# Performance work log

Measured on AMD Instinct MI355X. Metric: run time of the kernel, lower is better.

The kernel has to match this reference:

```python
import jax, jax.numpy as jnp
import numpy as np

DIM = 512; H = 56; W = 56; HEADS = 16; WS = 7; SHIFT = 3; MLP_RATIO = 4.0; B = 16
N = WS * WS              # tokens per window = 49
NW = (H // WS) * (W // WS)  # 64 windows
HID = int(DIM * MLP_RATIO)


def _rel_pos_index():
    coords = np.stack(np.meshgrid(np.arange(WS), np.arange(WS), indexing='ij')).reshape(2, -1)
    rel = (coords[:, :, None] - coords[:, None, :]).transpose(1, 2, 0)
    rel[..., 0] += WS - 1
    rel[..., 1] += WS - 1
    rel[..., 0] *= 2 * WS - 1
    return rel.sum(-1).astype(np.int32)  # (N, N)


def _attn_mask():
    # standard SW-MSA mask: 0 within same region, -100 across regions
    img = np.zeros((H, W), np.float32)
    cnt = 0
    sl = (slice(0, -WS), slice(-WS, -SHIFT), slice(-SHIFT, None))
    for hs in sl:
        for ws_ in sl:
            img[hs, ws_] = cnt
            cnt += 1
    mw = img.reshape(H // WS, WS, W // WS, WS).transpose(0, 2, 1, 3).reshape(-1, N)  # (NW, N)
    am = mw[:, None, :] - mw[:, :, None]
    return np.where(am != 0, np.float32(-100.0), np.float32(0.0))  # (NW, N, N)


def setup_inputs() -> dict:
    key = jax.random.key(0)
    ks = jax.random.split(key, 6)
    s = jnp.float32(0.02)
    return {
        'x': jax.random.normal(ks[0], (B, H * W, DIM), jnp.float32),
        'qkv_w': jax.random.normal(ks[1], (3 * DIM, DIM), jnp.float32) * s,  # layout (h dh 3) x C
        'qkv_b': jnp.zeros((3 * DIM,), jnp.float32),
        'out_w': jax.random.normal(ks[2], (DIM, DIM), jnp.float32) * s,
        'out_b': jnp.zeros((DIM,), jnp.float32),
        'rp_bias_table': jax.random.normal(ks[3], ((2 * WS - 1) ** 2, HEADS), jnp.float32) * s,
        'fc1_w': jax.random.normal(ks[4], (HID, DIM), jnp.float32) * s,
        'fc1_b': jnp.zeros((HID,), jnp.float32),
        'fc2_w': jax.random.normal(ks[5], (DIM, HID), jnp.float32) * s,
        'fc2_b': jnp.zeros((DIM,), jnp.float32),
        'ln1_w': jnp.ones((DIM,), jnp.float32),
        'ln1_b': jnp.zeros((DIM,), jnp.float32),
        'ln2_w': jnp.ones((DIM,), jnp.float32),
        'ln2_b': jnp.zeros((DIM,), jnp.float32),
        'attn_mask': jnp.asarray(_attn_mask()),
        'rp_index': jnp.asarray(_rel_pos_index()),
    }


def _ln(x, w, b):
    m = x.mean(-1, keepdims=True)
    v = ((x - m) ** 2).mean(-1, keepdims=True)
    return (x - m) * jax.lax.rsqrt(v + 1e-5) * w + b


def reference(x, qkv_w, qkv_b, out_w, out_b, rp_bias_table, fc1_w, fc1_b, fc2_w, fc2_b,
              ln1_w, ln1_b, ln2_w, ln2_b, attn_mask, rp_index):
    Bx, L, C = x.shape
    dh = C // HEADS
    scale = jnp.float32(dh) ** -0.5

    shortcut = x
    y = _ln(x, ln1_w, ln1_b).reshape(Bx, H, W, C)
    y = jnp.roll(y, (-SHIFT, -SHIFT), axis=(1, 2))
    # window partition -> (B*NW, N, C)
    xw = y.reshape(Bx, H // WS, WS, W // WS, WS, C).transpose(0, 1, 3, 2, 4, 5).reshape(-1, N, C)

    qkv = (xw @ qkv_w.T + qkv_b).reshape(-1, N, HEADS, dh, 3).transpose(4, 0, 2, 1, 3)
    q, k, v = qkv[0] * scale, qkv[1], qkv[2]          # (B_, h, N, dh)
    attn = jnp.einsum('bhnd,bhmd->bhnm', q, k)        # (B_, h, N, N)

    bias = rp_bias_table[rp_index.reshape(-1)].reshape(N, N, HEADS).transpose(2, 0, 1)
    attn = attn + 2.0 * bias                          # source adds the bias twice (faithful)
    attn = attn.reshape(Bx, NW, HEADS, N, N) + attn_mask[None, :, None]
    attn = jax.nn.softmax(attn, axis=-1).reshape(-1, HEADS, N, N)

    o = jnp.einsum('bhnm,bhmd->bhnd', attn, v).transpose(0, 2, 1, 3).reshape(-1, N, C)
    o = o @ out_w.T + out_b
    # window reverse + roll back
    o = o.reshape(Bx, H // WS, W // WS, WS, WS, C).transpose(0, 1, 3, 2, 4, 5).reshape(Bx, H, W, C)
    o = jnp.roll(o, (SHIFT, SHIFT), axis=(1, 2)).reshape(Bx, L, C)

    x = shortcut + o
    h2 = _ln(x, ln2_w, ln2_b)
    h2 = jax.nn.gelu(h2 @ fc1_w.T + fc1_b, approximate=False) @ fc2_w.T + fc2_b
    return x + h2
```

## Files before the change

kernel.cpp:

```cpp
#include <hip/hip_runtime.h>
#include <hip/hip_bf16.h>

#define CDIM 512
#define NHEADS 16
#define DH 32
#define NTOK 49
#define NWIN 64
#define BATCH 16
#define HH 56
#define WW 56
#define LTOK 3136
#define TTOK 50176
#define HID 2048
#define SHIFT_ 3

typedef short bf16x8 __attribute__((ext_vector_type(8)));
typedef float f32x4 __attribute__((ext_vector_type(4)));

__device__ __forceinline__ float b2f(unsigned int u) {
    return __uint_as_float((u & 0xffffu) << 16);
}
__device__ __forceinline__ unsigned short f2b(float f) {
    __hip_bfloat16 h = __float2bfloat16(f);
    return *reinterpret_cast<unsigned short*>(&h);
}
__device__ __forceinline__ void load8(const unsigned short* p, float* f) {
    uint4 r = *reinterpret_cast<const uint4*>(p);
    f[0] = b2f(r.x); f[1] = b2f(r.x >> 16);
    f[2] = b2f(r.y); f[3] = b2f(r.y >> 16);
    f[4] = b2f(r.z); f[5] = b2f(r.z >> 16);
    f[6] = b2f(r.w); f[7] = b2f(r.w >> 16);
}
__device__ __forceinline__ uint4 pack8(const float* f) {
    uint4 r;
    r.x = (unsigned)f2b(f[0]) | ((unsigned)f2b(f[1]) << 16);
    r.y = (unsigned)f2b(f[2]) | ((unsigned)f2b(f[3]) << 16);
    r.z = (unsigned)f2b(f[4]) | ((unsigned)f2b(f[5]) << 16);
    r.w = (unsigned)f2b(f[6]) | ((unsigned)f2b(f[7]) << 16);
    return r;
}
__device__ __forceinline__ bool probe_f32(const unsigned* p) { return p[0] == 0x3F800000u; }
__device__ __forceinline__ float ld1(const void* p, size_t i, bool f32) {
    return f32 ? ((const float*)p)[i] : b2f(((const unsigned short*)p)[i]);
}
__device__ __forceinline__ void load8_any(const void* p, size_t idx, bool f32, float* f) {
    if (f32) {
        const float4* q = (const float4*)((const float*)p + idx);
        float4 a = q[0], b = q[1];
        f[0]=a.x; f[1]=a.y; f[2]=a.z; f[3]=a.w; f[4]=b.x; f[5]=b.y; f[6]=b.z; f[7]=b.w;
    } else {
        load8((const unsigned short*)p + idx, f);
    }
}

#define GLOAD_LDS16(g, l) \
    __builtin_amdgcn_global_load_lds( \
        (const __attribute__((address_space(1))) unsigned int*)(g), \
        (__attribute__((address_space(3))) unsigned int*)(l), 16, 0, 0)

__global__ __launch_bounds__(256)
void cvt_kernel(const void* __restrict__ in, unsigned short* __restrict__ out,
                const unsigned* __restrict__ probe)
{
    bool f32in = probe_f32(probe);
    size_t idx = ((size_t)blockIdx.x * 256 + threadIdx.x) * 8;
    float f[8];
    load8_any(in, idx, f32in, f);
    *reinterpret_cast<uint4*>(out + idx) = pack8(f);
}

__global__ __launch_bounds__(256)
void cvt_qkvw_kernel(const void* __restrict__ in, unsigned short* __restrict__ out,
                     const unsigned* __restrict__ probe)
{
    bool f32in = probe_f32(probe);
    int r = blockIdx.x * 4 + (threadIdx.x >> 6);
    int lane = threadIdx.x & 63;
    int s = r >> 9, q = r & 511, h = q >> 5, d = q & 31;
    int orow = h * 96 + d * 3 + s;
    float f[8];
    load8_any(in, (size_t)orow * CDIM + lane * 8, f32in, f);
    *reinterpret_cast<uint4*>(out + (size_t)r * CDIM + lane * 8) = pack8(f);
}

__global__ __launch_bounds__(256)
void cmb_kernel(const void* __restrict__ rp_tab, const int* __restrict__ rp_idx,
                const void* __restrict__ mask, unsigned short* __restrict__ cmb,
                const unsigned* __restrict__ probe)
{
    bool f32in = probe_f32(probe);
    int wh = blockIdx.x;
    int wi = wh >> 4, h = wh & 15;
    for (int e = threadIdx.x; e < 4096; e += 256) {
        int q = e >> 6, k = e & 63;
        float v = -1e30f;
        if (q < NTOK && k < NTOK) {
            int bi = rp_idx[q * NTOK + k];
            v = 2.0f * ld1(rp_tab, (size_t)bi * NHEADS + h, f32in)
              + ld1(mask, (size_t)wi * NTOK * NTOK + (size_t)q * NTOK + k, f32in);
        }
        cmb[(size_t)wh * 4096 + e] = f2b(v);
    }
}

template<int SHIFTED, int XRAW>
__global__ __launch_bounds__(256)
void ln_kernel(const void* __restrict__ xin,
               const void* __restrict__ gw,
               const void* __restrict__ gb,
               unsigned short* __restrict__ out,
               const unsigned* __restrict__ probe)
{
    bool f32in = probe_f32(probe);
    int wid = threadIdx.x >> 6, lane = threadIdx.x & 63;
    int tok = blockIdx.x * 4 + wid;
    int c0 = lane * 8;
    float xs[8];
    load8_any(xin, (size_t)tok * CDIM + c0, XRAW && f32in, xs);
    float s = 0.f, s2 = 0.f;
#pragma unroll
    for (int j = 0; j < 8; ++j) { s += xs[j]; s2 += xs[j] * xs[j]; }
#pragma unroll
    for (int off = 32; off; off >>= 1) { s += __shfl_xor(s, off); s2 += __shfl_xor(s2, off); }
    float mean = s * (1.0f / CDIM);
    float var = s2 * (1.0f / CDIM) - mean * mean;
    float rstd = rsqrtf(var + 1e-5f);
    float wv[8], bv[8], ov[8];
    load8_any(gw, c0, f32in, wv);
    load8_any(gb, c0, f32in, bv);
#pragma unroll
    for (int j = 0; j < 8; ++j) ov[j] = (xs[j] - mean) * rstd * wv[j] + bv[j];
    size_t dst;
    if (SHIFTED) {
        int b = tok / LTOK, l = tok % LTOK;
        int h = l / WW, w = l % WW;
        int hs = (h + HH - SHIFT_) % HH;
        int ws_ = (w + WW - SHIFT_) % WW;
        int wh = hs / 7, ii = hs % 7, wwi = ws_ / 7, jj = ws_ % 7;
        int t = (b * NWIN + wh * 8 + wwi) * NTOK + ii * 7 + jj;
        dst = (size_t)t * CDIM + c0;
    } else {
        dst = (size_t)tok * CDIM + c0;
    }
    *reinterpret_cast<uint4*>(out + dst) = pack8(ov);
}

template<int EPI>
__global__ __launch_bounds__(256)
void gemm_kernel(const unsigned short* __restrict__ A,
                 const unsigned short* __restrict__ Wbf,
                 const void* __restrict__ bias,
                 const void* __restrict__ aux,
                 void* __restrict__ out0,
                 unsigned short* __restrict__ out1,
                 unsigned short* __restrict__ out2,
                 int K, int moff,
                 const unsigned* __restrict__ probe)
{
    bool f32in = probe_f32(probe);
    __shared__ __align__(16) unsigned short sA[2][128 * 32];
    __shared__ __align__(16) unsigned short sB[2][128 * 32];
    int tid = threadIdx.x;
    int wave = tid >> 6, lane = tid & 63, quad = lane >> 4, l16 = lane & 15;
    int bn = blockIdx.x, bm = blockIdx.y;
    int wm = (wave & 1) * 64, wn = (wave >> 1) * 64;

    const unsigned short* aP = A   + (size_t)(bm * 128 + (tid >> 2)) * K + (tid & 3) * 8;
    const unsigned short* bP = Wbf + (size_t)(bn * 128 + (tid >> 2)) * K + (tid & 3) * 8;
    const size_t rowhop = (size_t)64 * K;
    const int loff = tid * 16;

    f32x4 acc[16];
#pragma unroll
    for (int t = 0; t < 16; ++t) acc[t] = (f32x4){0.f, 0.f, 0.f, 0.f};

    GLOAD_LDS16(aP,          (char*)sA[0] + loff);
    GLOAD_LDS16(aP + rowhop, (char*)sA[0] + loff + 4096);
    GLOAD_LDS16(bP,          (char*)sB[0] + loff);
    GLOAD_LDS16(bP + rowhop, (char*)sB[0] + loff + 4096);
    __syncthreads();

    const int NT = K >> 5;
    int cur = 0;
    for (int t = 0; t < NT; ++t) {
        if (t + 1 < NT) {
            int k0 = (t + 1) << 5;
            char* dA = (char*)sA[cur ^ 1] + loff;
            char* dB = (char*)sB[cur ^ 1] + loff;
            GLOAD_LDS16(aP + k0,          dA);
            GLOAD_LDS16(aP + k0 + rowhop, dA + 4096);
            GLOAD_LDS16(bP + k0,          dB);
            GLOAD_LDS16(bP + k0 + rowhop, dB + 4096);
        }
        const unsigned short* cA = sA[cur];
        const unsigned short* cB = sB[cur];
        bf16x8 af[4], bfr[4];
#pragma unroll
        for (int am = 0; am < 4; ++am)
            af[am] = *reinterpret_cast<const bf16x8*>(&cA[(wm + am * 16 + l16) * 32 + quad * 8]);
#pragma unroll
        for (int bn_ = 0; bn_ < 4; ++bn_)
            bfr[bn_] = *reinterpret_cast<const bf16x8*>(&cB[(wn + bn_ * 16 + l16) * 32 + quad * 8]);
#pragma unroll
        for (int am = 0; am < 4; ++am)
#pragma unroll
            for (int bn_ = 0; bn_ < 4; ++bn_)
                acc[am * 4 + bn_] = __builtin_amdgcn_mfma_f32_16x16x32_bf16(
                    af[am], bfr[bn_], acc[am * 4 + bn_], 0, 0, 0);
        __syncthreads();
        cur ^= 1;
    }

#pragma unroll
    for (int bn_ = 0; bn_ < 4; ++bn_) {
        int gn = bn * 128 + wn + bn_ * 16 + l16;
        if (EPI == 0) {
            int s = gn >> 9, h = (gn >> 5) & 15, d = gn & 31;
            float bv = ld1(bias, h * 96 + d * 3 + s, f32in);
            unsigned short* outp = (s == 0) ? (unsigned short*)out0 : (s == 1 ? out1 : out2);
            float mul = (s == 0) ? 0.17677669529663687f : 1.0f;
#pragma unroll
            for (int am = 0; am < 4; ++am) {
#pragma unroll
                for (int r = 0; r < 4; ++r) {
                    int gm = bm * 128 + wm + am * 16 + quad * 4 + r;
                    int w = gm / NTOK, n = gm - w * NTOK;
                    size_t dst = ((size_t)(w * NHEADS + h) * NTOK + n) * DH + d;
                    outp[dst] = f2b((acc[am * 4 + bn_][r] + bv) * mul);
                }
            }
        } else {
            float bv = ld1(bias, gn, f32in);
#pragma unroll
            for (int am = 0; am < 4; ++am) {
#pragma unroll
                for (int r = 0; r < 4; ++r) {
                    int gm = bm * 128 + wm + am * 16 + quad * 4 + r;
                    float v = acc[am * 4 + bn_][r] + bv;
                    if (EPI == 1) {
                        int w = gm / NTOK, n = gm - w * NTOK;
                        int b = w >> 6, wi = w & 63;
                        int wh = wi >> 3, wwi = wi & 7;
                        int ii = n / 7, jj = n - ii * 7;
                        int h_ = (wh * 7 + ii + SHIFT_) % HH;
                        int w_ = (wwi * 7 + jj + SHIFT_) % WW;
                        size_t dst = ((size_t)b * LTOK + h_ * WW + w_) * CDIM + gn;
                        v += ld1(aux, dst, f32in);
                        ((unsigned short*)out0)[dst] = f2b(v);
                    } else if (EPI == 2) {
                        float g = 0.5f * v * (1.0f + erff(v * 0.70710678118654752f));
                        ((unsigned short*)out0)[(size_t)gm * HID + gn] = f2b(g);
                    } else {
                        size_t dst = (size_t)(moff + gm) * CDIM + gn;
                        v += b2f(((const unsigned short*)aux)[dst]);
                        if (f32in) ((float*)out0)[dst] = v;
                        else       ((unsigned short*)out0)[dst] = f2b(v);
                    }
                }
            }
        }
    }
}

__global__ __launch_bounds__(256)
void attn_kernel(const unsigned short* __restrict__ Qb,
                 const unsigned short* __restrict__ Kb,
                 const unsigned short* __restrict__ Vb,
                 const unsigned short* __restrict__ cmb,
                 unsigned short* __restrict__ Ob)
{
    __shared__ __align__(16) unsigned short Pl[4][64 * 72];
    int wid = threadIdx.x >> 6, lane = threadIdx.x & 63;
    int l16 = lane & 15, quad = lane >> 4;
    int wi = blockIdx.x >> 6, rem = blockIdx.x & 63;
    int b = rem >> 2, hq = rem & 3;
    int h = hq * 4 + wid;
    int bw = b * NWIN + wi;
    size_t base = (size_t)(bw * NHEADS + h) * (NTOK * DH);
    const unsigned short* cmbp = cmb + (size_t)(wi * NHEADS + h) * 4096;

    bf16x8 kf[4], qf[4];
#pragma unroll
    for (int t = 0; t < 4; ++t) {
        kf[t] = *reinterpret_cast<const bf16x8*>(Kb + base + (t * 16 + l16) * DH + quad * 8);
        qf[t] = *reinterpret_cast<const bf16x8*>(Qb + base + (t * 16 + l16) * DH + quad * 8);
    }
    f32x4 s[4][4];
#pragma unroll
    for (int kt = 0; kt < 4; ++kt)
#pragma unroll
        for (int nt = 0; nt < 4; ++nt)
            s[kt][nt] = (f32x4){0.f, 0.f, 0.f, 0.f};
#pragma unroll
    for (int kt = 0; kt < 4; ++kt)
#pragma unroll
        for (int nt = 0; nt < 4; ++nt)
            s[kt][nt] = __builtin_amdgcn_mfma_f32_16x16x32_bf16(kf[kt], qf[nt], s[kt][nt], 0, 0, 0);

    float mx[4] = {-1e30f, -1e30f, -1e30f, -1e30f}, sm[4] = {0.f, 0.f, 0.f, 0.f};
#pragma unroll
    for (int kt = 0; kt < 4; ++kt)
#pragma unroll
        for (int nt = 0; nt < 4; ++nt) {
            uint2 cv = *reinterpret_cast<const uint2*>(cmbp + (nt * 16 + l16) * 64 + kt * 16 + quad * 4);
            float c[4] = {b2f(cv.x), b2f(cv.x >> 16), b2f(cv.y), b2f(cv.y >> 16)};
#pragma unroll
            for (int r = 0; r < 4; ++r) {
                float sv = s[kt][nt][r] + c[r];
                s[kt][nt][r] = sv;
                mx[nt] = fmaxf(mx[nt], sv);
            }
        }
#pragma unroll
    for (int nt = 0; nt < 4; ++nt) {
        mx[nt] = fmaxf(mx[nt], __shfl_xor(mx[nt], 16));
        mx[nt] = fmaxf(mx[nt], __shfl_xor(mx[nt], 32));
    }
#pragma unroll
    for (int kt = 0; kt < 4; ++kt)
#pragma unroll
        for (int nt = 0; nt < 4; ++nt)
#pragma unroll
            for (int r = 0; r < 4; ++r) {
                float pv = expf(s[kt][nt][r] - mx[nt]);
                s[kt][nt][r] = pv;
                sm[nt] += pv;
            }
    float rs[4];
#pragma unroll
    for (int nt = 0; nt < 4; ++nt) {
        sm[nt] += __shfl_xor(sm[nt], 16);
        sm[nt] += __shfl_xor(sm[nt], 32);
        rs[nt] = 1.0f / sm[nt];
    }
    unsigned short* P = Pl[wid];
#pragma unroll
    for (int kt = 0; kt < 4; ++kt)
#pragma unroll
        for (int nt = 0; nt < 4; ++nt) {
            uint2 w;
            w.x = (unsigned)f2b(s[kt][nt][0] * rs[nt]) | ((unsigned)f2b(s[kt][nt][1] * rs[nt]) << 16);
            w.y = (unsigned)f2b(s[kt][nt][2] * rs[nt]) | ((unsigned)f2b(s[kt][nt][3] * rs[nt]) << 16);
            *reinterpret_cast<uint2*>(&P[(nt * 16 + l16) * 72 + kt * 16 + quad * 4]) = w;
        }

    f32x4 o[4][2];
#pragma unroll
    for (int mt = 0; mt < 4; ++mt)
#pragma unroll
        for (int n2 = 0; n2 < 2; ++n2)
            o[mt][n2] = (f32x4){0.f, 0.f, 0.f, 0.f};
#pragma unroll
    for (int ks = 0; ks < 2; ++ks) {
        bf16x8 pf[4];
#pragma unroll
        for (int mt = 0; mt < 4; ++mt)
            pf[mt] = *reinterpret_cast<const bf16x8*>(&P[(mt * 16 + l16) * 72 + ks * 32 + quad * 8]);
        bf16x8 vf[2];
#pragma unroll
        for (int n2 = 0; n2 < 2; ++n2) {
            union { bf16x8 v; unsigned short u[8]; } t;
#pragma unroll
            for (int j = 0; j < 8; ++j)
                t.u[j] = Vb[base + (size_t)(ks * 32 + quad * 8 + j) * DH + n2 * 16 + l16];
            vf[n2] = t.v;
        }
#pragma unroll
        for (int mt = 0; mt < 4; ++mt)
#pragma unroll
            for (int n2 = 0; n2 < 2; ++n2)
                o[mt][n2] = __builtin_amdgcn_mfma_f32_16x16x32_bf16(pf[mt], vf[n2], o[mt][n2], 0, 0, 0);
    }
#pragma unroll
    for (int mt = 0; mt < 4; ++mt)
#pragma unroll
        for (int n2 = 0; n2 < 2; ++n2)
#pragma unroll
            for (int r = 0; r < 4; ++r) {
                int q = mt * 16 + quad * 4 + r;
                if (q < NTOK)
                    Ob[((size_t)bw * NTOK + q) * CDIM + h * DH + n2 * 16 + l16] = f2b(o[mt][n2][r]);
            }
}

extern "C" void kernel_launch(void* const* d_in, const int* in_sizes, int n_in,
                              void* d_out, int out_size, void* d_ws, size_t ws_size,
                              hipStream_t stream)
{
    const void* x      = d_in[0];
    const void* qkv_w  = d_in[1];
    const void* qkv_b  = d_in[2];
    const void* out_w  = d_in[3];
    const void* out_b  = d_in[4];
    const void* rp_tab = d_in[5];
    const void* fc1_w  = d_in[6];
    const void* fc1_b  = d_in[7];
    const void* fc2_w  = d_in[8];
    const void* fc2_b  = d_in[9];
    const void* ln1_w  = d_in[10];
    const void* ln1_b  = d_in[11];
    const void* ln2_w  = d_in[12];
    const void* ln2_b  = d_in[13];
    const void* amask  = d_in[14];
    const int*  rp_idx = (const int*)d_in[15];
    const unsigned* probe = (const unsigned*)ln1_w;

    unsigned short* ws = (unsigned short*)d_ws;
    const size_t SZ = (size_t)TTOK * CDIM;
    unsigned short* xw = ws;
    unsigned short* Qb = ws + SZ;
    unsigned short* Kb = ws + 2 * SZ;
    unsigned short* Vb = ws + 3 * SZ;
    unsigned short* Ob = ws + 4 * SZ;
    unsigned short* Cmb = ws;
    unsigned short* X1 = ws;
    unsigned short* Hb = ws + SZ;
    unsigned short* fc1wbf = ws + 3 * SZ;
    unsigned short* fc2wbf = ws + 3 * SZ + (size_t)HID * CDIM;
    unsigned short* L2 = ws + 4 * SZ;
    unsigned short* qkvwbf = (unsigned short*)d_out;
    unsigned short* outwbf = qkvwbf + (size_t)3 * CDIM * CDIM;
    if (ws_size < 5 * SZ * sizeof(unsigned short)) return;

    const int HM = TTOK / 2;

    cvt_qkvw_kernel<<<(3 * CDIM) / 4, 256, 0, stream>>>(qkv_w, qkvwbf, probe);
    cvt_kernel<<<(CDIM * CDIM) / 2048, 256, 0, stream>>>(out_w, outwbf, probe);

    ln_kernel<1, 1><<<TTOK / 4, 256, 0, stream>>>(x, ln1_w, ln1_b, xw, probe);
    gemm_kernel<0><<<dim3((3 * CDIM) / 128, TTOK / 128), 256, 0, stream>>>(
        xw, qkvwbf, qkv_b, nullptr, Qb, Kb, Vb, CDIM, 0, probe);
    cmb_kernel<<<1024, 256, 0, stream>>>(rp_tab, rp_idx, amask, Cmb, probe);
    attn_kernel<<<4096, 256, 0, stream>>>(Qb, Kb, Vb, Cmb, Ob);

    cvt_kernel<<<(HID * CDIM) / 2048, 256, 0, stream>>>(fc1_w, fc1wbf, probe);
    cvt_kernel<<<(HID * CDIM) / 2048, 256, 0, stream>>>(fc2_w, fc2wbf, probe);

    gemm_kernel<1><<<dim3(CDIM / 128, TTOK / 128), 256, 0, stream>>>(
        Ob, outwbf, out_b, x, X1, nullptr, nullptr, CDIM, 0, probe);
    ln_kernel<0, 0><<<TTOK / 4, 256, 0, stream>>>(X1, ln2_w, ln2_b, L2, probe);

    for (int half = 0; half < 2; ++half) {
        size_t mo = (size_t)half * HM;
        gemm_kernel<2><<<dim3(HID / 128, HM / 128), 256, 0, stream>>>(
            L2 + mo * CDIM, fc1wbf, fc1_b, nullptr, Hb, nullptr, nullptr, CDIM, 0, probe);
        gemm_kernel<3><<<dim3(CDIM / 128, HM / 128), 256, 0, stream>>>(
            Hb, fc2wbf, fc2_b, X1, d_out, nullptr, nullptr, HID, (int)mo, probe);
    }
}
```

Before: 1.151 ms.

## Triple-buffer GEMM LDS loads with explicit vmcnt waits and swizzle workgroup order

Moves the GEMM main loop from double to triple buffering in LDS, so each iteration issues loads two K-tiles ahead. The full __syncthreads is replaced by inline s_waitcnt vmcnt(N) plus s_barrier, so only the oldest outstanding stage has to finish. It also remaps block indices so that consecutive workgroups are spread in groups of 8, likely to match the XCD round-robin dispatch and improve L2 locality. This uses more LDS per block, which may reduce occupancy. The hand-written vmcnt counts depend on each thread issuing exactly four loads per stage.

```diff
diff --git a/kernel.cpp b/kernel.cpp
--- a/kernel.cpp
+++ b/kernel.cpp
@@ -158,11 +158,18 @@
                  const unsigned* __restrict__ probe)
 {
     bool f32in = probe_f32(probe);
-    __shared__ __align__(16) unsigned short sA[2][128 * 32];
-    __shared__ __align__(16) unsigned short sB[2][128 * 32];
+    __shared__ __align__(16) unsigned short sA[3][128 * 32];
+    __shared__ __align__(16) unsigned short sB[3][128 * 32];
     int tid = threadIdx.x;
     int wave = tid >> 6, lane = tid & 63, quad = lane >> 4, l16 = lane & 15;
-    int bn = blockIdx.x, bm = blockIdx.y;
+
+    int nbn = gridDim.x;
+    int nwg = nbn * gridDim.y;
+    int wg = blockIdx.y * nbn + blockIdx.x;
+    int cpx = nwg >> 3;
+    int swz = (wg & 7) * cpx + (wg >> 3);
+    int bn = swz % nbn, bm = swz / nbn;
+
     int wm = (wave & 1) * 64, wn = (wave >> 1) * 64;
 
     const unsigned short* aP = A   + (size_t)(bm * 128 + (tid >> 2)) * K + (tid & 3) * 8;
@@ -174,23 +181,29 @@
 #pragma unroll
     for (int t = 0; t < 16; ++t) acc[t] = (f32x4){0.f, 0.f, 0.f, 0.f};
 
-    GLOAD_LDS16(aP,          (char*)sA[0] + loff);
-    GLOAD_LDS16(aP + rowhop, (char*)sA[0] + loff + 4096);
-    GLOAD_LDS16(bP,          (char*)sB[0] + loff);
-    GLOAD_LDS16(bP + rowhop, (char*)sB[0] + loff + 4096);
-    __syncthreads();
+#define STAGE(buf, k0) do { \
+        char* dA_ = (char*)sA[buf] + loff; \
+        char* dB_ = (char*)sB[buf] + loff; \
+        GLOAD_LDS16(aP + (k0),          dA_); \
+        GLOAD_LDS16(aP + (k0) + rowhop, dA_ + 4096); \
+        GLOAD_LDS16(bP + (k0),          dB_); \
+        GLOAD_LDS16(bP + (k0) + rowhop, dB_ + 4096); \
+    } while (0)
 
     const int NT = K >> 5;
+    STAGE(0, 0);
+    STAGE(1, 32);
+
     int cur = 0;
     for (int t = 0; t < NT; ++t) {
-        if (t + 1 < NT) {
-            int k0 = (t + 1) << 5;
-            char* dA = (char*)sA[cur ^ 1] + loff;
-            char* dB = (char*)sB[cur ^ 1] + loff;
-            GLOAD_LDS16(aP + k0,          dA);
-            GLOAD_LDS16(aP + k0 + rowhop, dA + 4096);
-            GLOAD_LDS16(bP + k0,          dB);
-            GLOAD_LDS16(bP + k0 + rowhop, dB + 4096);
+        if (t + 2 < NT) {
+            int nb = cur + 2; if (nb >= 3) nb -= 3;
+            STAGE(nb, (t + 2) << 5);
+            asm volatile("s_waitcnt vmcnt(8)\n\ts_barrier" ::: "memory");
+        } else if (t + 2 == NT) {
+            asm volatile("s_waitcnt vmcnt(4)\n\ts_barrier" ::: "memory");
+        } else {
+            asm volatile("s_waitcnt vmcnt(0)\n\ts_barrier" ::: "memory");
         }
         const unsigned short* cA = sA[cur];
         const unsigned short* cB = sB[cur];
@@ -207,9 +220,10 @@
             for (int bn_ = 0; bn_ < 4; ++bn_)
                 acc[am * 4 + bn_] = __builtin_amdgcn_mfma_f32_16x16x32_bf16(
                     af[am], bfr[bn_], acc[am * 4 + bn_], 0, 0, 0);
-        __syncthreads();
-        cur ^= 1;
-    }
+        asm volatile("s_barrier" ::: "memory");
+        cur += 1; if (cur >= 3) cur -= 3;
+    }
+#undef STAGE
 
 #pragma unroll
     for (int bn_ = 0; bn_ < 4; ++bn_) {
```

New measurement: 1.075 ms. -6.6%, faster.

## Enlarge GEMM tiles to 256x256 with 512 threads, swizzled LDS and XCD remap

Applied to the files above, without the earlier changes.

Rewrites the shared bf16 GEMM kernel to use 256x256 output tiles with 8 waves, a 64-wide K step and a 128 KB double-buffered LDS stage. LDS columns are XOR-swizzled so fragment reads avoid bank conflicts. Block indices are remapped so neighbouring tiles land on the same XCD, improving L2 reuse. The goal is more operand reuse and fewer barriers per FLOP. The cost is far fewer blocks: the fc2 GEMM launches fewer blocks than there are CUs, and the out-projection GEMM has a poor tail. The large accumulator set also raises register pressure.

```diff
diff --git a/kernel.cpp b/kernel.cpp
--- a/kernel.cpp
+++ b/kernel.cpp
@@ -146,7 +146,7 @@
 }
 
 template<int EPI>
-__global__ __launch_bounds__(256)
+__global__ __launch_bounds__(512, 2)
 void gemm_kernel(const unsigned short* __restrict__ A,
                  const unsigned short* __restrict__ Wbf,
                  const void* __restrict__ bias,
@@ -158,85 +158,97 @@
                  const unsigned* __restrict__ probe)
 {
     bool f32in = probe_f32(probe);
-    __shared__ __align__(16) unsigned short sA[2][128 * 32];
-    __shared__ __align__(16) unsigned short sB[2][128 * 32];
+    __shared__ __align__(16) char lds[131072];
     int tid = threadIdx.x;
     int wave = tid >> 6, lane = tid & 63, quad = lane >> 4, l16 = lane & 15;
-    int bn = blockIdx.x, bm = blockIdx.y;
-    int wm = (wave & 1) * 64, wn = (wave >> 1) * 64;
-
-    const unsigned short* aP = A   + (size_t)(bm * 128 + (tid >> 2)) * K + (tid & 3) * 8;
-    const unsigned short* bP = Wbf + (size_t)(bn * 128 + (tid >> 2)) * K + (tid & 3) * 8;
-    const size_t rowhop = (size_t)64 * K;
-    const int loff = tid * 16;
-
-    f32x4 acc[16];
-#pragma unroll
-    for (int t = 0; t < 16; ++t) acc[t] = (f32x4){0.f, 0.f, 0.f, 0.f};
-
-    GLOAD_LDS16(aP,          (char*)sA[0] + loff);
-    GLOAD_LDS16(aP + rowhop, (char*)sA[0] + loff + 4096);
-    GLOAD_LDS16(bP,          (char*)sB[0] + loff);
-    GLOAD_LDS16(bP + rowhop, (char*)sB[0] + loff + 4096);
+
+    int nbn = gridDim.x;
+    int nwg = nbn * gridDim.y;
+    int wg = blockIdx.y * nbn + blockIdx.x;
+    int q8 = nwg >> 3, r8 = nwg & 7;
+    int xcd = wg & 7, lin = wg >> 3;
+    int swz = (xcd < r8 ? xcd * (q8 + 1) : r8 * (q8 + 1) + (xcd - r8) * q8) + lin;
+    int bn = swz % nbn, bm = swz / nbn;
+
+    int wm = (wave >> 2) * 128;
+    int wn = (wave & 3) * 64;
+
+    int arow = tid >> 3;
+    int scol = (((tid & 7) ^ ((tid >> 3) & 7)) << 3);
+    const unsigned short* aP = A   + (size_t)(bm * 256 + arow) * K + scol;
+    const unsigned short* bP = Wbf + (size_t)(bn * 256 + arow) * K + scol;
+
+    f32x4 acc[32];
+#pragma unroll
+    for (int t = 0; t < 32; ++t) acc[t] = (f32x4){0.f, 0.f, 0.f, 0.f};
+
+#define STAGE(bufoff, k0) do { \
+        char* dA_ = lds + (bufoff) + tid * 16; \
+        char* dB_ = dA_ + 32768; \
+        _Pragma("unroll") \
+        for (int p_ = 0; p_ < 4; ++p_) { \
+            GLOAD_LDS16(aP + (size_t)p_ * 64 * K + (k0), dA_ + p_ * 8192); \
+            GLOAD_LDS16(bP + (size_t)p_ * 64 * K + (k0), dB_ + p_ * 8192); \
+        } \
+    } while (0)
+
+    const int NT = K >> 6;
+    STAGE(0, 0);
     __syncthreads();
 
-    const int NT = K >> 5;
     int cur = 0;
     for (int t = 0; t < NT; ++t) {
-        if (t + 1 < NT) {
-            int k0 = (t + 1) << 5;
-            char* dA = (char*)sA[cur ^ 1] + loff;
-            char* dB = (char*)sB[cur ^ 1] + loff;
-            GLOAD_LDS16(aP + k0,          dA);
-            GLOAD_LDS16(aP + k0 + rowhop, dA + 4096);
-            GLOAD_LDS16(bP + k0,          dB);
-            GLOAD_LDS16(bP + k0 + rowhop, dB + 4096);
-        }
-        const unsigned short* cA = sA[cur];
-        const unsigned short* cB = sB[cur];
-        bf16x8 af[4], bfr[4];
-#pragma unroll
-        for (int am = 0; am < 4; ++am)
-            af[am] = *reinterpret_cast<const bf16x8*>(&cA[(wm + am * 16 + l16) * 32 + quad * 8]);
-#pragma unroll
-        for (int bn_ = 0; bn_ < 4; ++bn_)
-            bfr[bn_] = *reinterpret_cast<const bf16x8*>(&cB[(wn + bn_ * 16 + l16) * 32 + quad * 8]);
-#pragma unroll
-        for (int am = 0; am < 4; ++am)
-#pragma unroll
-            for (int bn_ = 0; bn_ < 4; ++bn_)
-                acc[am * 4 + bn_] = __builtin_amdgcn_mfma_f32_16x16x32_bf16(
-                    af[am], bfr[bn_], acc[am * 4 + bn_], 0, 0, 0);
+        if (t + 1 < NT) STAGE((cur ^ 1) << 16, (t + 1) << 6);
+        const unsigned short* cA = (const unsigned short*)(lds + (cur << 16));
+        const unsigned short* cB = (const unsigned short*)(lds + (cur << 16) + 32768);
+#pragma unroll
+        for (int ks = 0; ks < 2; ++ks) {
+            int swzc = (((ks << 2) + quad) ^ (l16 & 7)) << 3;
+            bf16x8 af[8], bfr[4];
+#pragma unroll
+            for (int am = 0; am < 8; ++am)
+                af[am] = *reinterpret_cast<const bf16x8*>(&cA[(wm + am * 16 + l16) * 64 + swzc]);
+#pragma unroll
+            for (int j = 0; j < 4; ++j)
+                bfr[j] = *reinterpret_cast<const bf16x8*>(&cB[(wn + j * 16 + l16) * 64 + swzc]);
+#pragma unroll
+            for (int am = 0; am < 8; ++am)
+#pragma unroll
+                for (int j = 0; j < 4; ++j)
+                    acc[am * 4 + j] = __builtin_amdgcn_mfma_f32_16x16x32_bf16(
+                        af[am], bfr[j], acc[am * 4 + j], 0, 0, 0);
+        }
         __syncthreads();
         cur ^= 1;
     }
-
-#pragma unroll
-    for (int bn_ = 0; bn_ < 4; ++bn_) {
-        int gn = bn * 128 + wn + bn_ * 16 + l16;
+#undef STAGE
+
+#pragma unroll
+    for (int j = 0; j < 4; ++j) {
+        int gn = bn * 256 + wn + j * 16 + l16;
         if (EPI == 0) {
             int s = gn >> 9, h = (gn >> 5) & 15, d = gn & 31;
             float bv = ld1(bias, h * 96 + d * 3 + s, f32in);
             unsigned short* outp = (s == 0) ? (unsigned short*)out0 : (s == 1 ? out1 : out2);
             float mul = (s == 0) ? 0.17677669529663687f : 1.0f;
 #pragma unroll
-            for (int am = 0; am < 4; ++am) {
+            for (int am = 0; am < 8; ++am) {
 #pragma unroll
                 for (int r = 0; r < 4; ++r) {
-                    int gm = bm * 128 + wm + am * 16 + quad * 4 + r;
+                    int gm = bm * 256 + wm + am * 16 + quad * 4 + r;
                     int w = gm / NTOK, n = gm - w * NTOK;
                     size_t dst = ((size_t)(w * NHEADS + h) * NTOK + n) * DH + d;
-                    outp[dst] = f2b((acc[am * 4 + bn_][r] + bv) * mul);
+                    outp[dst] = f2b((acc[am * 4 + j][r] + bv) * mul);
                 }
             }
         } else {
             float bv = ld1(bias, gn, f32in);
 #pragma unroll
-            for (int am = 0; am < 4; ++am) {
+            for (int am = 0; am < 8; ++am) {
 #pragma unroll
                 for (int r = 0; r < 4; ++r) {
-                    int gm = bm * 128 + wm + am * 16 + quad * 4 + r;
-                    float v = acc[am * 4 + bn_][r] + bv;
+                    int gm = bm * 256 + wm + am * 16 + quad * 4 + r;
+                    float v = acc[am * 4 + j][r] + bv;
                     if (EPI == 1) {
                         int w = gm / NTOK, n = gm - w * NTOK;
                         int b = w >> 6, wi = w & 63;
@@ -428,7 +440,7 @@
     cvt_kernel<<<(CDIM * CDIM) / 2048, 256, 0, stream>>>(out_w, outwbf, probe);
 
     ln_kernel<1, 1><<<TTOK / 4, 256, 0, stream>>>(x, ln1_w, ln1_b, xw, probe);
-    gemm_kernel<0><<<dim3((3 * CDIM) / 128, TTOK / 128), 256, 0, stream>>>(
+    gemm_kernel<0><<<dim3((3 * CDIM) / 256, TTOK / 256), 512, 0, stream>>>(
         xw, qkvwbf, qkv_b, nullptr, Qb, Kb, Vb, CDIM, 0, probe);
     cmb_kernel<<<1024, 256, 0, stream>>>(rp_tab, rp_idx, amask, Cmb, probe);
     attn_kernel<<<4096, 256, 0, stream>>>(Qb, Kb, Vb, Cmb, Ob);
@@ -436,15 +448,15 @@
     cvt_kernel<<<(HID * CDIM) / 2048, 256, 0, stream>>>(fc1_w, fc1wbf, probe);
     cvt_kernel<<<(HID * CDIM) / 2048, 256, 0, stream>>>(fc2_w, fc2wbf, probe);
 
-    gemm_kernel<1><<<dim3(CDIM / 128, TTOK / 128), 256, 0, stream>>>(
+    gemm_kernel<1><<<dim3(CDIM / 256, TTOK / 256), 512, 0, stream>>>(
         Ob, outwbf, out_b, x, X1, nullptr, nullptr, CDIM, 0, probe);
     ln_kernel<0, 0><<<TTOK / 4, 256, 0, stream>>>(X1, ln2_w, ln2_b, L2, probe);
 
     for (int half = 0; half < 2; ++half) {
         size_t mo = (size_t)half * HM;
-        gemm_kernel<2><<<dim3(HID / 128, HM / 128), 256, 0, stream>>>(
+        gemm_kernel<2><<<dim3(HID / 256, HM / 256), 512, 0, stream>>>(
             L2 + mo * CDIM, fc1wbf, fc1_b, nullptr, Hb, nullptr, nullptr, CDIM, 0, probe);
-        gemm_kernel<3><<<dim3(CDIM / 128, HM / 128), 256, 0, stream>>>(
+        gemm_kernel<3><<<dim3(CDIM / 256, HM / 256), 512, 0, stream>>>(
             Hb, fc2wbf, fc2_b, X1, d_out, nullptr, nullptr, HID, (int)mo, probe);
     }
 }
```

New measurement: 1.044 ms. 9.3% less time.
